# Kernel optimization log

Measured on AMD Instinct MI355X. Metric: run time of the kernel, lower is better.

The kernel has to match this reference:

```python
import jax, jax.numpy as jnp
import numpy as np

HEADS = 20  # SDXL-style: hidden_size 1280 / head_dim 64
IP_SCALE = 1.0


def setup_inputs() -> dict:
    key = jax.random.key(0)
    ks = jax.random.split(key, 12)
    B, Sq, T, C, D, NIP = 4, 4096, 77, 1280, 2048, 16
    s = lambda fan: 1.0 / np.sqrt(fan)
    # post-softmax multiplicative mask: col 0 (sot token) forced to 1, rest a binary spatial mask
    spat = (jax.random.uniform(ks[0], (1, Sq, 1)) < 0.5).astype(jnp.float32)
    attention_mask = jnp.concatenate([jnp.ones((1, Sq, 1)), jnp.tile(spat, (1, 1, T - 1))], axis=-1)
    return {
        "hidden_states": jax.random.normal(ks[1], (B, Sq, C), jnp.float32),
        "encoder_hidden_states": jax.random.normal(ks[2], (B, T, D), jnp.float32),
        "ip_hidden_states": jax.random.normal(ks[3], (B, NIP, D), jnp.float32),
        "attention_mask": attention_mask,
        "Wq": jax.random.normal(ks[4], (C, C), jnp.float32) * s(C),
        "Wk": jax.random.normal(ks[5], (D, C), jnp.float32) * s(D),
        "Wv": jax.random.normal(ks[6], (D, C), jnp.float32) * s(D),
        "Wo": jax.random.normal(ks[7], (C, C), jnp.float32) * s(C),
        "bo": jnp.zeros((C,), jnp.float32),
        "Wk_ip": jax.random.normal(ks[8], (D, C), jnp.float32) * s(D),
        "Wv_ip": jax.random.normal(ks[9], (D, C), jnp.float32) * s(D),
    }


def reference(hidden_states, encoder_hidden_states, ip_hidden_states, attention_mask,
              Wq, Wk, Wv, Wo, bo, Wk_ip, Wv_ip):
    B, Sq, C = hidden_states.shape
    H = HEADS
    d = C // H
    scale = d ** -0.5
    # projections (torch Linear with weights stored [in, out])
    q = (hidden_states @ Wq).reshape(B, Sq, H, d)
    k = (encoder_hidden_states @ Wk).reshape(B, -1, H, d)
    v = (encoder_hidden_states @ Wv).reshape(B, -1, H, d)
    # explicit QK^T softmax, then POST-softmax multiplicative mask (as in get_attention_scores + mask multiply)
    scores = jnp.einsum('bqhd,bkhd->bhqk', q, k) * scale
    probs = jax.nn.softmax(scores, axis=-1)
    probs = probs * attention_mask[:, None, :, :]  # [1,1,Sq,T] broadcast over batch*heads
    out = jnp.einsum('bhqk,bkhd->bqhd', probs, v).reshape(B, Sq, C)
    out = out @ Wo + bo  # to_out[0]; to_out[1] is dropout (identity at eval)
    # IP-adapter stream (single stream, no spatial ip mask): standard SDPA against ip tokens
    k_ip = (ip_hidden_states @ Wk_ip).reshape(B, -1, H, d)
    v_ip = (ip_hidden_states @ Wv_ip).reshape(B, -1, H, d)
    s_ip = jnp.einsum('bqhd,bkhd->bhqk', q, k_ip) * scale
    p_ip = jax.nn.softmax(s_ip, axis=-1)
    ip_out = jnp.einsum('bhqk,bkhd->bqhd', p_ip, v_ip).reshape(B, Sq, C)
    return out + IP_SCALE * ip_out
```

## Files before the change

### kernel.cpp

```cpp
#include <hip/hip_runtime.h>

typedef __attribute__((ext_vector_type(4))) float f32x4;
typedef __attribute__((ext_vector_type(8))) short s16x8;
typedef __attribute__((ext_vector_type(8))) __bf16 bf16x8;
typedef unsigned short u16;

__device__ __forceinline__ u16 f2b(float f) {
  union { float f; unsigned u; } x; x.f = f;
  unsigned r = x.u + 0x7fffu + ((x.u >> 16) & 1u);
  return (u16)(r >> 16);
}
__device__ __forceinline__ float b2f(u16 u) {
  union { unsigned u; float f; } x; x.u = ((unsigned)u) << 16;
  return x.f;
}
__device__ __forceinline__ void gld16(const void* g, void* l) {
  __builtin_amdgcn_global_load_lds(
      (const __attribute__((address_space(1))) unsigned int*)g,
      (__attribute__((address_space(3))) unsigned int*)l, 16, 0, 0);
}
__device__ __forceinline__ f32x4 mfma_bf16(s16x8 a, s16x8 b, f32x4 c) {
  return __builtin_amdgcn_mfma_f32_16x16x32_bf16(
      __builtin_bit_cast(bf16x8, a), __builtin_bit_cast(bf16x8, b), c, 0, 0, 0);
}

#define BAR() asm volatile("s_barrier" ::: "memory")

__global__ void k_convert_all(const float* __restrict__ hs, const float* __restrict__ ehs,
                              const float* __restrict__ iph,
                              u16* __restrict__ hsb, u16* __restrict__ ehsb,
                              u16* __restrict__ ipb) {
  const int n1 = 16384 * 1280 / 4, n2 = 308 * 2048 / 4, n3 = 64 * 2048 / 4;
  int i = blockIdx.x * blockDim.x + threadIdx.x;
  const float* src; u16* dst; int j = i;
  if (i < n1) { src = hs; dst = hsb; }
  else if (i < n1 + n2) { src = ehs; dst = ehsb; j = i - n1; }
  else if (i < n1 + n2 + n3) { src = iph; dst = ipb; j = i - n1 - n2; }
  else return;
  float4 v = ((const float4*)src)[j];
  ushort4 o;
  o.x = f2b(v.x); o.y = f2b(v.y); o.z = f2b(v.z); o.w = f2b(v.w);
  ((ushort4*)dst)[j] = o;
}

__device__ __forceinline__ void transpose_tile(const float* __restrict__ W,
                                               u16* __restrict__ WT, int K, int N) {
  __shared__ float tile[32][33];
  int n0 = blockIdx.x * 32, k0 = blockIdx.y * 32;
  int tx = threadIdx.x & 31, ty = threadIdx.x >> 5;
#pragma unroll
  for (int i = 0; i < 32; i += 8)
    tile[ty + i][tx] = W[(size_t)(k0 + ty + i) * N + n0 + tx];
  __syncthreads();
#pragma unroll
  for (int i = 0; i < 32; i += 8)
    WT[(size_t)(n0 + ty + i) * K + k0 + tx] = f2b(tile[tx][ty + i]);
}

__global__ void k_transpose4(const float* W0, const float* W1, const float* W2,
                             const float* W3, u16* T0, u16* T1, u16* T2, u16* T3,
                             int K, int N) {
  int z = blockIdx.z;
  const float* W = (z == 0) ? W0 : (z == 1) ? W1 : (z == 2) ? W2 : W3;
  u16* T = (z == 0) ? T0 : (z == 1) ? T1 : (z == 2) ? T2 : T3;
  transpose_tile(W, T, K, N);
}
__global__ void k_transpose2(const float* W0, const float* W1, u16* T0, u16* T1,
                             int K, int N) {
  int z = blockIdx.z;
  transpose_tile(z ? W1 : W0, z ? T1 : T0, K, N);
}

__device__ __forceinline__ void gemm_core0(
    const u16* __restrict__ A, const u16* __restrict__ BT,
    int M, int N, int K, u16* __restrict__ outb, int m0, int n0) {
  const int tid = threadIdx.x;
  const int l = tid & 63;
  const int w = tid >> 6;
  const int wr = w >> 1, wc = w & 1;
  __shared__ u16 As[128 * 32];
  __shared__ u16 Bs[128 * 32];
  f32x4 acc[4][4] = {};

  const int o0 = tid * 16;
  const int o1 = o0 + 4096;
  const int ra0 = o0 >> 6, ca0 = (o0 & 63) >> 1;
  const int ra1 = o1 >> 6, ca1 = (o1 & 63) >> 1;
  int ga0 = m0 + ra0; if (ga0 >= M) ga0 = M - 1;
  int ga1 = m0 + ra1; if (ga1 >= M) ga1 = M - 1;
  const u16* Ar0 = A + (size_t)ga0 * K + ca0;
  const u16* Ar1 = A + (size_t)ga1 * K + ca1;
  const u16* Br0 = BT + (size_t)(n0 + ra0) * K + ca0;
  const u16* Br1 = BT + (size_t)(n0 + ra1) * K + ca1;

  for (int k0 = 0; k0 < K; k0 += 32) {
    gld16(Ar0 + k0, &As[o0 >> 1]);
    gld16(Ar1 + k0, &As[o1 >> 1]);
    gld16(Br0 + k0, &Bs[o0 >> 1]);
    gld16(Br1 + k0, &Bs[o1 >> 1]);
    __syncthreads();
    s16x8 af[4], bfr[4];
#pragma unroll
    for (int mi = 0; mi < 4; ++mi)
      af[mi] = *(const s16x8*)&As[(wr * 64 + mi * 16 + (l & 15)) * 32 + (l >> 4) * 8];
#pragma unroll
    for (int ni = 0; ni < 4; ++ni)
      bfr[ni] = *(const s16x8*)&Bs[(wc * 64 + ni * 16 + (l & 15)) * 32 + (l >> 4) * 8];
#pragma unroll
    for (int mi = 0; mi < 4; ++mi)
#pragma unroll
      for (int ni = 0; ni < 4; ++ni)
        acc[mi][ni] = mfma_bf16(af[mi], bfr[ni], acc[mi][ni]);
    __syncthreads();
  }

#pragma unroll
  for (int mi = 0; mi < 4; ++mi) {
    const int mbase = m0 + wr * 64 + mi * 16 + (l >> 4) * 4;
#pragma unroll
    for (int ni = 0; ni < 4; ++ni) {
      const int ncol = n0 + wc * 64 + ni * 16 + (l & 15);
#pragma unroll
      for (int r = 0; r < 4; ++r) {
        int m = mbase + r;
        if (m < M) outb[(size_t)m * N + ncol] = f2b(acc[mi][ni][r]);
      }
    }
  }
}

__global__ __launch_bounds__(256) void k_gemm_small4(
    const u16* __restrict__ ehsb, const u16* __restrict__ ipb,
    const u16* __restrict__ WkT, const u16* __restrict__ WvT,
    const u16* __restrict__ WkipT, const u16* __restrict__ WvipT,
    u16* kbuf, u16* vbuf, u16* kipb, u16* vipb) {
  const int z = blockIdx.z;
  const int M = (z < 2) ? 308 : 64;
  const int m0 = blockIdx.y * 128;
  if (m0 >= M) return;
  const u16* A = (z < 2) ? ehsb : ipb;
  const u16* BT = (z == 0) ? WkT : (z == 1) ? WvT : (z == 2) ? WkipT : WvipT;
  u16* out = (z == 0) ? kbuf : (z == 1) ? vbuf : (z == 2) ? kipb : vipb;
  gemm_core0(A, BT, M, 1280, 2048, out, m0, blockIdx.x * 128);
}

template <int EPI>
__global__ __launch_bounds__(512, 1) void k_gemm256(
    const u16* __restrict__ A, const u16* __restrict__ BT,
    int N, int K, float alpha,
    u16* __restrict__ outb, float* __restrict__ outf,
    const float* __restrict__ bias, const u16* __restrict__ ipadd,
    int nbx) {
  __shared__ u16 lds[73728];
  const int tid = threadIdx.x, l = tid & 63, w = tid >> 6;
  const int lr = l & 15, lg = l >> 4;
  const int wr = w >> 2, wc = w & 3;
  const bool wlo = (w < 4);

  const int nwg = gridDim.x;
  const int q = nwg >> 3, r = nwg & 7;
  const int xcd = blockIdx.x & 7, lid = blockIdx.x >> 3;
  const int wg = (xcd < r) ? (xcd * (q + 1) + lid)
                           : (r * (q + 1) + (xcd - r) * q + lid);
  const int bm0 = (wg / nbx) * 256, bn0 = (wg % nbx) * 320;

  const int srow = tid >> 2;
  const int sslot = ((tid & 3) ^ ((srow >> 1) & 3)) * 8;
  const size_t aO0 = (size_t)(bm0 + srow) * K + sslot;
  const size_t aO1 = aO0 + (size_t)128 * K;
  const size_t bO0 = (size_t)(bn0 + srow) * K + sslot;
  const size_t bO1 = bO0 + (size_t)128 * K;
  const size_t bO2 = bO0 + (size_t)256 * K;
  const int d0 = tid * 8, d1 = (tid + 512) * 8, d2 = (tid + 1024) * 8;

  const int KT = K >> 6;
  f32x4 acc[8][5] = {};
  s16x8 bfv[5], afv[4];

  const int xsw = (lg ^ ((lr >> 1) & 3)) * 8;
  const int aRow = (wr * 128 + lr) * 32 + xsw;
  const int bRow = 32768 + (wc * 80 + lr) * 32 + xsw;

#define STAGE_A(buf, kk, kt)                                           \
  {                                                                    \
    const int base_ = (buf) * 16384 + (kk) * 8192;                     \
    const size_t go_ = (size_t)(kt) * 64 + (kk) * 32;                  \
    gld16(A + aO0 + go_, &lds[base_ + d0]);                            \
    gld16(A + aO1 + go_, &lds[base_ + d1]);                            \
  }
#define STAGE_B(buf, kk, kt)                                           \
  {                                                                    \
    const int base_ = 32768 + (buf) * 20480 + (kk) * 10240;            \
    const size_t go_ = (size_t)(kt) * 64 + (kk) * 32;                  \
    gld16(BT + bO0 + go_, &lds[base_ + d0]);                           \
    gld16(BT + bO1 + go_, &lds[base_ + d1]);                           \
    if (wlo) gld16(BT + bO2 + go_, &lds[base_ + d2]);                  \
  }
#define WAITVM()                                                       \
  {                                                                    \
    if (wlo) asm volatile("s_waitcnt vmcnt(5)" ::: "memory");          \
    else     asm volatile("s_waitcnt vmcnt(4)" ::: "memory");          \
  }
#define WAITVM0() asm volatile("s_waitcnt vmcnt(0)" ::: "memory")

  STAGE_A(0, 0, 0);
  STAGE_B(0, 0, 0);
  STAGE_A(0, 1, 0);
  STAGE_B(0, 1, 0);
  WAITVM();
  BAR();

  int cur = 0;
  for (int j = 0; j < KT; ++j) {
    const int nx = cur ^ 1;
    const int ab = cur * 16384;
    const int bb = cur * 20480;
    const bool pf = (j + 1 < KT);
#pragma unroll
    for (int ni = 0; ni < 5; ++ni)
      bfv[ni] = *(const s16x8*)&lds[bb + bRow + ni * 512];
#pragma unroll
    for (int mi = 0; mi < 4; ++mi)
      afv[mi] = *(const s16x8*)&lds[ab + aRow + mi * 512];
    if (pf) STAGE_A(nx, 0, j + 1);
    __builtin_amdgcn_s_setprio(1);
#pragma unroll
    for (int mi = 0; mi < 4; ++mi)
#pragma unroll
      for (int ni = 0; ni < 5; ++ni)
        acc[mi][ni] = mfma_bf16(afv[mi], bfv[ni], acc[mi][ni]);
    __builtin_amdgcn_s_setprio(0);
    BAR();
#pragma unroll
    for (int mi = 0; mi < 4; ++mi)
      afv[mi] = *(const s16x8*)&lds[ab + aRow + (mi + 4) * 512];
    if (pf) STAGE_B(nx, 0, j + 1);
    __builtin_amdgcn_s_setprio(1);
#pragma unroll
    for (int mi = 0; mi < 4; ++mi)
#pragma unroll
      for (int ni = 0; ni < 5; ++ni)
        acc[mi + 4][ni] = mfma_bf16(afv[mi], bfv[ni], acc[mi + 4][ni]);
    __builtin_amdgcn_s_setprio(0);
    if (pf) { WAITVM(); } else { WAITVM0(); }
    BAR();
#pragma unroll
    for (int ni = 0; ni < 5; ++ni)
      bfv[ni] = *(const s16x8*)&lds[bb + 10240 + bRow + ni * 512];
#pragma unroll
    for (int mi = 0; mi < 4; ++mi)
      afv[mi] = *(const s16x8*)&lds[ab + 8192 + aRow + mi * 512];
    if (pf) STAGE_A(nx, 1, j + 1);
    __builtin_amdgcn_s_setprio(1);
#pragma unroll
    for (int mi = 0; mi < 4; ++mi)
#pragma unroll
      for (int ni = 0; ni < 5; ++ni)
        acc[mi][ni] = mfma_bf16(afv[mi], bfv[ni], acc[mi][ni]);
    __builtin_amdgcn_s_setprio(0);
    BAR();
#pragma unroll
    for (int mi = 0; mi < 4; ++mi)
      afv[mi] = *(const s16x8*)&lds[ab + 8192 + aRow + (mi + 4) * 512];
    if (pf) STAGE_B(nx, 1, j + 1);
    __builtin_amdgcn_s_setprio(1);
#pragma unroll
    for (int mi = 0; mi < 4; ++mi)
#pragma unroll
      for (int ni = 0; ni < 5; ++ni)
        acc[mi + 4][ni] = mfma_bf16(afv[mi], bfv[ni], acc[mi + 4][ni]);
    __builtin_amdgcn_s_setprio(0);
    if (pf) { WAITVM(); } else { WAITVM0(); }
    BAR();
    cur = nx;
  }

  WAITVM0();
  __syncthreads();

  if constexpr (EPI == 0) {
#pragma unroll
    for (int half = 0; half < 2; ++half) {
      if (half) __syncthreads();
      if (wr == half) {
#pragma unroll
        for (int mi = 0; mi < 8; ++mi) {
          const int row = mi * 16 + lg * 4;
#pragma unroll
          for (int ni = 0; ni < 5; ++ni) {
            const int col = wc * 80 + ni * 16 + lr;
#pragma unroll
            for (int rr = 0; rr < 4; ++rr)
              lds[(row + rr) * 320 + col] = f2b(acc[mi][ni][rr] * alpha);
          }
        }
      }
      __syncthreads();
      const int rrow = tid >> 2;
#pragma unroll
      for (int jj = 0; jj < 10; ++jj) {
        const int ch = (tid & 3) + jj * 4;
        *(int4*)(outb + (size_t)(bm0 + half * 128 + rrow) * N + bn0 + ch * 8) =
            *(const int4*)&lds[rrow * 320 + ch * 8];
      }
    }
  } else {
#pragma unroll
    for (int mi = 0; mi < 8; ++mi) {
      const int mrow = bm0 + wr * 128 + mi * 16 + lg * 4;
#pragma unroll
      for (int ni = 0; ni < 5; ++ni) {
        const int ncol = bn0 + wc * 80 + ni * 16 + lr;
#pragma unroll
        for (int rr = 0; rr < 4; ++rr) {
          const size_t idx = (size_t)(mrow + rr) * N + ncol;
          outf[idx] = acc[mi][ni][rr] + bias[ncol] + b2f(ipadd[idx]);
        }
      }
    }
  }
#undef STAGE_A
#undef STAGE_B
#undef WAITVM
#undef WAITVM0
}

__global__ __launch_bounds__(512, 4) void k_attn(
    const u16* __restrict__ Q,
    const u16* __restrict__ Kb,
    const u16* __restrict__ Vb,
    const u16* __restrict__ Kip,
    const u16* __restrict__ Vip,
    const float* __restrict__ mask,
    u16* __restrict__ Oattn,
    u16* __restrict__ Oip) {
  const int qt = blockIdx.x, h = blockIdx.y, b = blockIdx.z;
  const int tid = threadIdx.x, l = tid & 63, w = tid >> 6;
  const int lr = l & 15, lg = l >> 4;
  const int r0 = w * 16;
  const int m0 = b * 4096 + qt * 128;

  __shared__ u16 KV[192][72];
  __shared__ u16 Ps[128][104];
  __shared__ u16 P2s[128][40];

  const u16* qrow = Q + (size_t)(m0 + r0 + lr) * 1280 + h * 64;
  s16x8 aq0 = *(const s16x8*)(qrow + lg * 8);
  s16x8 aq1 = *(const s16x8*)(qrow + 32 + lg * 8);

  for (int s = tid; s < 192 * 8; s += 512) {
    const int row = s >> 3, seg = s & 7;
    int4 v = {0, 0, 0, 0};
    const u16* src = nullptr;
    if (row < 77)       src = Kb  + (size_t)(b * 77 + row) * 1280 + h * 64 + seg * 8;
    else if (row < 80)  src = nullptr;
    else if (row < 96)  src = Kip + (size_t)(b * 16 + row - 80) * 1280 + h * 64 + seg * 8;
    else if (row < 173) src = Vb  + (size_t)(b * 77 + row - 96) * 1280 + h * 64 + seg * 8;
    else if (row < 176) src = nullptr;
    else                src = Vip + (size_t)(b * 16 + row - 176) * 1280 + h * 64 + seg * 8;
    if (src) v = *(const int4*)src;
    *(int4*)&KV[row][(seg ^ ((row >> 3) & 3)) * 8] = v;
  }
  __syncthreads();

  f32x4 sc[5];
  f32x4 sip = {};
#pragma unroll
  for (int t5 = 0; t5 < 6; ++t5) {
    const int trow = t5 * 16 + lr;
    const int qz = (trow >> 3) & 3;
    s16x8 b0 = *(const s16x8*)&KV[trow][(lg ^ qz) * 8];
    s16x8 b1 = *(const s16x8*)&KV[trow][((lg + 4) ^ qz) * 8];
    f32x4 c = {};
    c = mfma_bf16(aq0, b0, c);
    c = mfma_bf16(aq1, b1, c);
    if (t5 < 5) sc[t5] = c; else sip = c;
  }

#pragma unroll
  for (int r = 0; r < 4; ++r) {
    float mx = fmaxf(fmaxf(fmaxf(sc[0][r], sc[1][r]), fmaxf(sc[2][r], sc[3][r])), sc[4][r]);
    mx = fmaxf(mx, __shfl_xor(mx, 1));
    mx = fmaxf(mx, __shfl_xor(mx, 2));
    mx = fmaxf(mx, __shfl_xor(mx, 4));
    mx = fmaxf(mx, __shfl_xor(mx, 8));
    float p[5], sm = 0.f;
#pragma unroll
    for (int t5 = 0; t5 < 5; ++t5) {
      bool valid = (t5 < 4) | (lr < 13);
      p[t5] = valid ? __expf(sc[t5][r] - mx) : 0.f;
      sm += p[t5];
    }
    sm += __shfl_xor(sm, 1);
    sm += __shfl_xor(sm, 2);
    sm += __shfl_xor(sm, 4);
    sm += __shfl_xor(sm, 8);
    const float inv = 1.0f / sm;
    const int row = r0 + lg * 4 + r;
    const int qg = qt * 128 + row;
#pragma unroll
    for (int t5 = 0; t5 < 5; ++t5) {
      int t = t5 * 16 + lr;
      float pf = 0.f;
      if (t < 77) pf = p[t5] * inv * mask[qg * 77 + t];
      Ps[row][t] = f2b(pf);
    }
    Ps[row][80 + lr] = 0;

    float m2 = sip[r];
    m2 = fmaxf(m2, __shfl_xor(m2, 1));
    m2 = fmaxf(m2, __shfl_xor(m2, 2));
    m2 = fmaxf(m2, __shfl_xor(m2, 4));
    m2 = fmaxf(m2, __shfl_xor(m2, 8));
    float pi = __expf(sip[r] - m2);
    float s2 = pi;
    s2 += __shfl_xor(s2, 1);
    s2 += __shfl_xor(s2, 2);
    s2 += __shfl_xor(s2, 4);
    s2 += __shfl_xor(s2, 8);
    P2s[row][lr] = 0;
    P2s[row][16 + lr] = f2b(pi / s2);
  }

  s16x8 ap[3];
#pragma unroll
  for (int ks = 0; ks < 3; ++ks)
    ap[ks] = *(const s16x8*)&Ps[r0 + lr][ks * 32 + lg * 8];
  s16x8 aip = *(const s16x8*)&P2s[r0 + lr][lg * 8];

  f32x4 om[4], oi[4];
#pragma unroll
  for (int nt = 0; nt < 4; ++nt) {
    const int dcol = (nt * 16 + lr) ^ (lg << 3);
    f32x4 o = {};
#pragma unroll
    for (int ks = 0; ks < 3; ++ks) {
      s16x8 bv;
#pragma unroll
      for (int j = 0; j < 8; ++j)
        bv[j] = (short)KV[96 + ks * 32 + lg * 8 + j][dcol];
      o = mfma_bf16(ap[ks], bv, o);
    }
    s16x8 bip;
#pragma unroll
    for (int j = 0; j < 8; ++j)
      bip[j] = (short)KV[160 + lg * 8 + j][dcol];
    f32x4 o2 = {};
    o2 = mfma_bf16(aip, bip, o2);
    om[nt] = o;
    oi[nt] = o2;
  }

  __syncthreads();

  u16 (*Om)[72] = (u16(*)[72]) & KV[0][0];
  u16 (*Oi)[72] = (u16(*)[72]) & Ps[0][0];
#pragma unroll
  for (int nt = 0; nt < 4; ++nt)
#pragma unroll
    for (int r = 0; r < 4; ++r) {
      const int row = r0 + lg * 4 + r;
      const int d = nt * 16 + lr;
      Om[row][d] = f2b(om[nt][r]);
      Oi[row][d] = f2b(oi[nt][r]);
    }
  __syncthreads();

  for (int s = tid; s < 128 * 8; s += 512) {
    const int row = s >> 3, seg = s & 7;
    const size_t g = (size_t)(m0 + row) * 1280 + h * 64 + seg * 8;
    *(int4*)(Oattn + g) = *(const int4*)&Om[row][seg * 8];
    *(int4*)(Oip + g) = *(const int4*)&Oi[row][seg * 8];
  }
}

extern "C" void kernel_launch(void* const* d_in, const int* in_sizes, int n_in,
                              void* d_out, int out_size, void* d_ws, size_t ws_size,
                              hipStream_t stream) {
  (void)in_sizes; (void)n_in; (void)out_size; (void)ws_size;
  const float* hs   = (const float*)d_in[0];
  const float* ehs  = (const float*)d_in[1];
  const float* iph  = (const float*)d_in[2];
  const float* mask = (const float*)d_in[3];
  const float* Wq   = (const float*)d_in[4];
  const float* Wk   = (const float*)d_in[5];
  const float* Wv   = (const float*)d_in[6];
  const float* Wo   = (const float*)d_in[7];
  const float* bo   = (const float*)d_in[8];
  const float* Wkip = (const float*)d_in[9];
  const float* Wvip = (const float*)d_in[10];
  float* out = (float*)d_out;

  char* ws = (char*)d_ws;
  size_t off = 0;
  auto alloc = [&](size_t bytes) {
    char* p = ws + off;
    off += (bytes + 255) & ~(size_t)255;
    return p;
  };
  u16* hsb   = (u16*)alloc(16384ull * 1280 * 2);
  u16* qbuf  = (u16*)alloc(16384ull * 1280 * 2);
  u16* ipout = (u16*)alloc(16384ull * 1280 * 2);
  u16* WqT   = (u16*)alloc(1280ull * 1280 * 2);
  u16* WoT   = (u16*)alloc(1280ull * 1280 * 2);
  u16* WkT   = (u16*)alloc(1280ull * 2048 * 2);
  u16* WvT   = (u16*)alloc(1280ull * 2048 * 2);
  u16* WkipT = (u16*)alloc(1280ull * 2048 * 2);
  u16* WvipT = (u16*)alloc(1280ull * 2048 * 2);
  u16* ehsb  = (u16*)alloc(308ull * 2048 * 2);
  u16* ipb   = (u16*)alloc(64ull * 2048 * 2);
  u16* kbuf  = (u16*)alloc(308ull * 1280 * 2);
  u16* vbuf  = (u16*)alloc(308ull * 1280 * 2);
  u16* kipb  = (u16*)alloc(64ull * 1280 * 2);
  u16* vipb  = (u16*)alloc(64ull * 1280 * 2);

  const int ntot4 = (16384 * 1280 + 308 * 2048 + 64 * 2048) / 4;
  k_convert_all<<<(ntot4 + 255) / 256, 256, 0, stream>>>(hs, ehs, iph, hsb, ehsb, ipb);
  k_transpose4<<<dim3(40, 64, 4), 256, 0, stream>>>(Wk, Wv, Wkip, Wvip,
                                                    WkT, WvT, WkipT, WvipT, 2048, 1280);
  k_transpose2<<<dim3(40, 40, 2), 256, 0, stream>>>(Wq, Wo, WqT, WoT, 1280, 1280);

  k_gemm256<0><<<256, 512, 0, stream>>>(hsb, WqT, 1280, 1280, 0.125f,
                                        qbuf, nullptr, nullptr, nullptr, 4);
  k_gemm_small4<<<dim3(10, 3, 4), 256, 0, stream>>>(ehsb, ipb, WkT, WvT, WkipT, WvipT,
                                                    kbuf, vbuf, kipb, vipb);

  k_attn<<<dim3(32, 20, 4), 512, 0, stream>>>(qbuf, kbuf, vbuf, kipb, vipb, mask,
                                              hsb, ipout);

  k_gemm256<1><<<256, 512, 0, stream>>>(hsb, WoT, 1280, 1280, 1.f,
                                        nullptr, out, bo, ipout, 4);
}
```

Baseline: 266.3 us.

## Deepen GEMM pipeline to four-slot ring with three-ahead prefetch, coalesce epilogue stores

Restructures the GEMM main loop from a double-buffered 64-wide K step (two 32-wide halves) into a four-slot ring of 32-wide K tiles, with prefetch three tiles ahead and vmcnt waits adjusted for the deeper pipeline. This keeps more global loads in flight to hide memory latency, at the cost of one barrier per 32-wide K step and more outstanding loads per wave. It also remaps the bf16 epilogue store so each row is written by eight threads over wider contiguous segments, aiming for better write coalescing.

```diff
diff --git a/kernel.cpp b/kernel.cpp
--- a/kernel.cpp
+++ b/kernel.cpp
@@ -173,7 +173,7 @@
   const size_t bO2 = bO0 + (size_t)256 * K;
   const int d0 = tid * 8, d1 = (tid + 512) * 8, d2 = (tid + 1024) * 8;
 
-  const int KT = K >> 6;
+  const int KT = K >> 5;
   f32x4 acc[8][5] = {};
   s16x8 bfv[5], afv[4];
 
@@ -181,48 +181,52 @@
   const int aRow = (wr * 128 + lr) * 32 + xsw;
   const int bRow = 32768 + (wc * 80 + lr) * 32 + xsw;
 
-#define STAGE_A(buf, kk, kt)                                           \
+#define STAGE_A(slot, kt)                                              \
   {                                                                    \
-    const int base_ = (buf) * 16384 + (kk) * 8192;                     \
-    const size_t go_ = (size_t)(kt) * 64 + (kk) * 32;                  \
+    const int base_ = (slot) * 8192;                                   \
+    const size_t go_ = (size_t)(kt) * 32;                              \
     gld16(A + aO0 + go_, &lds[base_ + d0]);                            \
     gld16(A + aO1 + go_, &lds[base_ + d1]);                            \
   }
-#define STAGE_B(buf, kk, kt)                                           \
+#define STAGE_B(slot, kt)                                              \
   {                                                                    \
-    const int base_ = 32768 + (buf) * 20480 + (kk) * 10240;            \
-    const size_t go_ = (size_t)(kt) * 64 + (kk) * 32;                  \
+    const int base_ = 32768 + (slot) * 10240;                          \
+    const size_t go_ = (size_t)(kt) * 32;                              \
     gld16(BT + bO0 + go_, &lds[base_ + d0]);                           \
     gld16(BT + bO1 + go_, &lds[base_ + d1]);                           \
     if (wlo) gld16(BT + bO2 + go_, &lds[base_ + d2]);                  \
   }
-#define WAITVM()                                                       \
+#define WAIT_DEEP()                                                    \
+  {                                                                    \
+    if (wlo) asm volatile("s_waitcnt vmcnt(10)" ::: "memory");         \
+    else     asm volatile("s_waitcnt vmcnt(8)" ::: "memory");          \
+  }
+#define WAIT_MID()                                                     \
   {                                                                    \
     if (wlo) asm volatile("s_waitcnt vmcnt(5)" ::: "memory");          \
     else     asm volatile("s_waitcnt vmcnt(4)" ::: "memory");          \
   }
 #define WAITVM0() asm volatile("s_waitcnt vmcnt(0)" ::: "memory")
 
-  STAGE_A(0, 0, 0);
-  STAGE_B(0, 0, 0);
-  STAGE_A(0, 1, 0);
-  STAGE_B(0, 1, 0);
-  WAITVM();
+  STAGE_A(0, 0); STAGE_B(0, 0);
+  STAGE_A(1, 1); STAGE_B(1, 1);
+  STAGE_A(2, 2); STAGE_B(2, 2);
+  WAIT_DEEP();
   BAR();
 
-  int cur = 0;
   for (int j = 0; j < KT; ++j) {
-    const int nx = cur ^ 1;
-    const int ab = cur * 16384;
-    const int bb = cur * 20480;
-    const bool pf = (j + 1 < KT);
+    const int slot = j & 3;
+    const int ab = slot * 8192;
+    const int bb = slot * 10240;
+    const bool pf = (j + 3 < KT);
+    const int s3 = (j + 3) & 3;
 #pragma unroll
     for (int ni = 0; ni < 5; ++ni)
       bfv[ni] = *(const s16x8*)&lds[bb + bRow + ni * 512];
 #pragma unroll
     for (int mi = 0; mi < 4; ++mi)
       afv[mi] = *(const s16x8*)&lds[ab + aRow + mi * 512];
-    if (pf) STAGE_A(nx, 0, j + 1);
+    if (pf) STAGE_A(s3, j + 3);
     __builtin_amdgcn_s_setprio(1);
 #pragma unroll
     for (int mi = 0; mi < 4; ++mi)
@@ -234,7 +238,7 @@
 #pragma unroll
     for (int mi = 0; mi < 4; ++mi)
       afv[mi] = *(const s16x8*)&lds[ab + aRow + (mi + 4) * 512];
-    if (pf) STAGE_B(nx, 0, j + 1);
+    if (pf) STAGE_B(s3, j + 3);
     __builtin_amdgcn_s_setprio(1);
 #pragma unroll
     for (int mi = 0; mi < 4; ++mi)
@@ -242,37 +246,10 @@
       for (int ni = 0; ni < 5; ++ni)
         acc[mi + 4][ni] = mfma_bf16(afv[mi], bfv[ni], acc[mi + 4][ni]);
     __builtin_amdgcn_s_setprio(0);
-    if (pf) { WAITVM(); } else { WAITVM0(); }
+    if (pf) { WAIT_DEEP(); }
+    else if (j == KT - 3) { WAIT_MID(); }
+    else { WAITVM0(); }
     BAR();
-#pragma unroll
-    for (int ni = 0; ni < 5; ++ni)
-      bfv[ni] = *(const s16x8*)&lds[bb + 10240 + bRow + ni * 512];
-#pragma unroll
-    for (int mi = 0; mi < 4; ++mi)
-      afv[mi] = *(const s16x8*)&lds[ab + 8192 + aRow + mi * 512];
-    if (pf) STAGE_A(nx, 1, j + 1);
-    __builtin_amdgcn_s_setprio(1);
-#pragma unroll
-    for (int mi = 0; mi < 4; ++mi)
-#pragma unroll
-      for (int ni = 0; ni < 5; ++ni)
-        acc[mi][ni] = mfma_bf16(afv[mi], bfv[ni], acc[mi][ni]);
-    __builtin_amdgcn_s_setprio(0);
-    BAR();
-#pragma unroll
-    for (int mi = 0; mi < 4; ++mi)
-      afv[mi] = *(const s16x8*)&lds[ab + 8192 + aRow + (mi + 4) * 512];
-    if (pf) STAGE_B(nx, 1, j + 1);
-    __builtin_amdgcn_s_setprio(1);
-#pragma unroll
-    for (int mi = 0; mi < 4; ++mi)
-#pragma unroll
-      for (int ni = 0; ni < 5; ++ni)
-        acc[mi + 4][ni] = mfma_bf16(afv[mi], bfv[ni], acc[mi + 4][ni]);
-    __builtin_amdgcn_s_setprio(0);
-    if (pf) { WAITVM(); } else { WAITVM0(); }
-    BAR();
-    cur = nx;
   }
 
   WAITVM0();
@@ -296,13 +273,17 @@
         }
       }
       __syncthreads();
-      const int rrow = tid >> 2;
-#pragma unroll
-      for (int jj = 0; jj < 10; ++jj) {
-        const int ch = (tid & 3) + jj * 4;
-        *(int4*)(outb + (size_t)(bm0 + half * 128 + rrow) * N + bn0 + ch * 8) =
-            *(const int4*)&lds[rrow * 320 + ch * 8];
-      }
+      const int rbase = tid >> 3;
+      const int cseg = tid & 7;
+#pragma unroll
+      for (int rr2 = 0; rr2 < 2; ++rr2)
+#pragma unroll
+        for (int jj = 0; jj < 5; ++jj) {
+          const int row = rr2 * 64 + rbase;
+          const int ch = cseg + jj * 8;
+          *(int4*)(outb + (size_t)(bm0 + half * 128 + row) * N + bn0 + ch * 8) =
+              *(const int4*)&lds[row * 320 + ch * 8];
+        }
     }
   } else {
 #pragma unroll
@@ -321,7 +302,8 @@
   }
 #undef STAGE_A
 #undef STAGE_B
-#undef WAITVM
+#undef WAIT_DEEP
+#undef WAIT_MID
 #undef WAITVM0
 }
 
```

Result: no change. 266.4 us (+0.0%).

## Restructure 256x320 GEMM main loop with 64-wide K slabs and register double-buffering

Applied to the files above, without the earlier changes.

Reworks the large GEMM's K loop. Each iteration now stages a full 64-wide K slab (XOR-swizzled 8-chunk rows) into one of two LDS buffers and issues it once. Fragments are register double-buffered with explicit lgkmcnt waits and sched_barriers, so only one block barrier runs per K step instead of four. The epilogue store pattern is also changed to 8 threads per row for wider coalesced writes. The intent is to cut barrier and synchronisation overhead and overlap LDS reads with MFMA. The trade-off is more register pressure, a full vmcnt(0) wait per step, and 32-bit offsets that could overflow for large operands.

```diff
diff --git a/kernel.cpp b/kernel.cpp
--- a/kernel.cpp
+++ b/kernel.cpp
@@ -155,7 +155,6 @@
   const int tid = threadIdx.x, l = tid & 63, w = tid >> 6;
   const int lr = l & 15, lg = l >> 4;
   const int wr = w >> 2, wc = w & 3;
-  const bool wlo = (w < 4);
 
   const int nwg = gridDim.x;
   const int q = nwg >> 3, r = nwg & 7;
@@ -164,118 +163,108 @@
                            : (r * (q + 1) + (xcd - r) * q + lid);
   const int bm0 = (wg / nbx) * 256, bn0 = (wg % nbx) * 320;
 
-  const int srow = tid >> 2;
-  const int sslot = ((tid & 3) ^ ((srow >> 1) & 3)) * 8;
-  const size_t aO0 = (size_t)(bm0 + srow) * K + sslot;
-  const size_t aO1 = aO0 + (size_t)128 * K;
-  const size_t bO0 = (size_t)(bn0 + srow) * K + sslot;
-  const size_t bO1 = bO0 + (size_t)128 * K;
-  const size_t bO2 = bO0 + (size_t)256 * K;
-  const int d0 = tid * 8, d1 = (tid + 512) * 8, d2 = (tid + 1024) * 8;
+  const int srow = tid >> 3;
+  const int scol = ((tid & 7) ^ (srow & 7)) * 8;
+  const int aOff0 = (bm0 + srow) * K + scol;
+  const int bOff0 = (bn0 + srow) * K + scol;
+  const int dD = tid * 8;
 
   const int KT = K >> 6;
   f32x4 acc[8][5] = {};
-  s16x8 bfv[5], afv[4];
-
-  const int xsw = (lg ^ ((lr >> 1) & 3)) * 8;
-  const int aRow = (wr * 128 + lr) * 32 + xsw;
-  const int bRow = 32768 + (wc * 80 + lr) * 32 + xsw;
-
-#define STAGE_A(buf, kk, kt)                                           \
-  {                                                                    \
-    const int base_ = (buf) * 16384 + (kk) * 8192;                     \
-    const size_t go_ = (size_t)(kt) * 64 + (kk) * 32;                  \
-    gld16(A + aO0 + go_, &lds[base_ + d0]);                            \
-    gld16(A + aO1 + go_, &lds[base_ + d1]);                            \
-  }
-#define STAGE_B(buf, kk, kt)                                           \
-  {                                                                    \
-    const int base_ = 32768 + (buf) * 20480 + (kk) * 10240;            \
-    const size_t go_ = (size_t)(kt) * 64 + (kk) * 32;                  \
-    gld16(BT + bO0 + go_, &lds[base_ + d0]);                           \
-    gld16(BT + bO1 + go_, &lds[base_ + d1]);                           \
-    if (wlo) gld16(BT + bO2 + go_, &lds[base_ + d2]);                  \
-  }
-#define WAITVM()                                                       \
-  {                                                                    \
-    if (wlo) asm volatile("s_waitcnt vmcnt(5)" ::: "memory");          \
-    else     asm volatile("s_waitcnt vmcnt(4)" ::: "memory");          \
-  }
-#define WAITVM0() asm volatile("s_waitcnt vmcnt(0)" ::: "memory")
-
-  STAGE_A(0, 0, 0);
-  STAGE_B(0, 0, 0);
-  STAGE_A(0, 1, 0);
-  STAGE_B(0, 1, 0);
-  WAITVM();
+
+  const int xs0 = (lg ^ (lr & 7)) * 8;
+  const int xs1 = ((4 + lg) ^ (lr & 7)) * 8;
+  const int aR = (wr * 128 + lr) * 64;
+  const int bR = 16384 + (wc * 80 + lr) * 64;
+
+#define SB0() __builtin_amdgcn_sched_barrier(0)
+#define LGKM(n) asm volatile("s_waitcnt lgkmcnt(" #n ")" ::: "memory")
+#define VMW0() asm volatile("s_waitcnt vmcnt(0)" ::: "memory")
+#define STAGE(slotu, kt)                                                \
+  {                                                                     \
+    const int sb_ = (slotu);                                            \
+    const int ko_ = (kt) * 64;                                          \
+    _Pragma("unroll")                                                   \
+    for (int i_ = 0; i_ < 4; ++i_)                                      \
+      gld16(A + aOff0 + i_ * 64 * K + ko_, &lds[sb_ + dD + i_ * 4096]); \
+    _Pragma("unroll")                                                   \
+    for (int i_ = 0; i_ < 5; ++i_)                                      \
+      gld16(BT + bOff0 + i_ * 64 * K + ko_,                             \
+            &lds[sb_ + 16384 + dD + i_ * 4096]);                        \
+  }
+
+  STAGE(0, 0);
+  VMW0();
   BAR();
 
-  int cur = 0;
+  s16x8 afvA[4], afvB[4], bfvA[5], bfvB[5];
   for (int j = 0; j < KT; ++j) {
-    const int nx = cur ^ 1;
-    const int ab = cur * 16384;
-    const int bb = cur * 20480;
+    const int sb = (j & 1) * 36864;
+    const int nsb = 36864 - sb;
     const bool pf = (j + 1 < KT);
 #pragma unroll
+    for (int mi = 0; mi < 4; ++mi)
+      afvA[mi] = *(const s16x8*)&lds[sb + aR + mi * 1024 + xs0];
+#pragma unroll
     for (int ni = 0; ni < 5; ++ni)
-      bfv[ni] = *(const s16x8*)&lds[bb + bRow + ni * 512];
-#pragma unroll
-    for (int mi = 0; mi < 4; ++mi)
-      afv[mi] = *(const s16x8*)&lds[ab + aRow + mi * 512];
-    if (pf) STAGE_A(nx, 0, j + 1);
+      bfvA[ni] = *(const s16x8*)&lds[sb + bR + ni * 1024 + xs0];
+    SB0();
+#pragma unroll
+    for (int mi = 0; mi < 4; ++mi)
+      afvB[mi] = *(const s16x8*)&lds[sb + aR + (mi + 4) * 1024 + xs0];
+    SB0();
+    LGKM(4); SB0();
     __builtin_amdgcn_s_setprio(1);
 #pragma unroll
     for (int mi = 0; mi < 4; ++mi)
 #pragma unroll
       for (int ni = 0; ni < 5; ++ni)
-        acc[mi][ni] = mfma_bf16(afv[mi], bfv[ni], acc[mi][ni]);
+        acc[mi][ni] = mfma_bf16(afvA[mi], bfvA[ni], acc[mi][ni]);
     __builtin_amdgcn_s_setprio(0);
+    SB0();
+#pragma unroll
+    for (int mi = 0; mi < 4; ++mi)
+      afvA[mi] = *(const s16x8*)&lds[sb + aR + mi * 1024 + xs1];
+#pragma unroll
+    for (int ni = 0; ni < 5; ++ni)
+      bfvB[ni] = *(const s16x8*)&lds[sb + bR + ni * 1024 + xs1];
+    SB0();
+    LGKM(9); SB0();
+    __builtin_amdgcn_s_setprio(1);
+#pragma unroll
+    for (int mi = 0; mi < 4; ++mi)
+#pragma unroll
+      for (int ni = 0; ni < 5; ++ni)
+        acc[mi + 4][ni] = mfma_bf16(afvB[mi], bfvA[ni], acc[mi + 4][ni]);
+    __builtin_amdgcn_s_setprio(0);
+    SB0();
+#pragma unroll
+    for (int mi = 0; mi < 4; ++mi)
+      afvB[mi] = *(const s16x8*)&lds[sb + aR + (mi + 4) * 1024 + xs1];
+    SB0();
+    if (pf) STAGE(nsb, j + 1);
+    SB0();
+    LGKM(4); SB0();
+    __builtin_amdgcn_s_setprio(1);
+#pragma unroll
+    for (int mi = 0; mi < 4; ++mi)
+#pragma unroll
+      for (int ni = 0; ni < 5; ++ni)
+        acc[mi][ni] = mfma_bf16(afvA[mi], bfvB[ni], acc[mi][ni]);
+    __builtin_amdgcn_s_setprio(0);
+    SB0();
+    LGKM(0); SB0();
+    __builtin_amdgcn_s_setprio(1);
+#pragma unroll
+    for (int mi = 0; mi < 4; ++mi)
+#pragma unroll
+      for (int ni = 0; ni < 5; ++ni)
+        acc[mi + 4][ni] = mfma_bf16(afvB[mi], bfvB[ni], acc[mi + 4][ni]);
+    __builtin_amdgcn_s_setprio(0);
+    if (pf) VMW0();
     BAR();
-#pragma unroll
-    for (int mi = 0; mi < 4; ++mi)
-      afv[mi] = *(const s16x8*)&lds[ab + aRow + (mi + 4) * 512];
-    if (pf) STAGE_B(nx, 0, j + 1);
-    __builtin_amdgcn_s_setprio(1);
-#pragma unroll
-    for (int mi = 0; mi < 4; ++mi)
-#pragma unroll
-      for (int ni = 0; ni < 5; ++ni)
-        acc[mi + 4][ni] = mfma_bf16(afv[mi], bfv[ni], acc[mi + 4][ni]);
-    __builtin_amdgcn_s_setprio(0);
-    if (pf) { WAITVM(); } else { WAITVM0(); }
-    BAR();
-#pragma unroll
-    for (int ni = 0; ni < 5; ++ni)
-      bfv[ni] = *(const s16x8*)&lds[bb + 10240 + bRow + ni * 512];
-#pragma unroll
-    for (int mi = 0; mi < 4; ++mi)
-      afv[mi] = *(const s16x8*)&lds[ab + 8192 + aRow + mi * 512];
-    if (pf) STAGE_A(nx, 1, j + 1);
-    __builtin_amdgcn_s_setprio(1);
-#pragma unroll
-    for (int mi = 0; mi < 4; ++mi)
-#pragma unroll
-      for (int ni = 0; ni < 5; ++ni)
-        acc[mi][ni] = mfma_bf16(afv[mi], bfv[ni], acc[mi][ni]);
-    __builtin_amdgcn_s_setprio(0);
-    BAR();
-#pragma unroll
-    for (int mi = 0; mi < 4; ++mi)
-      afv[mi] = *(const s16x8*)&lds[ab + 8192 + aRow + (mi + 4) * 512];
-    if (pf) STAGE_B(nx, 1, j + 1);
-    __builtin_amdgcn_s_setprio(1);
-#pragma unroll
-    for (int mi = 0; mi < 4; ++mi)
-#pragma unroll
-      for (int ni = 0; ni < 5; ++ni)
-        acc[mi + 4][ni] = mfma_bf16(afv[mi], bfv[ni], acc[mi + 4][ni]);
-    __builtin_amdgcn_s_setprio(0);
-    if (pf) { WAITVM(); } else { WAITVM0(); }
-    BAR();
-    cur = nx;
-  }
-
-  WAITVM0();
+  }
+
   __syncthreads();
 
   if constexpr (EPI == 0) {
@@ -296,13 +285,17 @@
         }
       }
       __syncthreads();
-      const int rrow = tid >> 2;
-#pragma unroll
-      for (int jj = 0; jj < 10; ++jj) {
-        const int ch = (tid & 3) + jj * 4;
-        *(int4*)(outb + (size_t)(bm0 + half * 128 + rrow) * N + bn0 + ch * 8) =
-            *(const int4*)&lds[rrow * 320 + ch * 8];
-      }
+      const int rbase = tid >> 3;
+      const int cseg = tid & 7;
+#pragma unroll
+      for (int rr2 = 0; rr2 < 2; ++rr2)
+#pragma unroll
+        for (int jj = 0; jj < 5; ++jj) {
+          const int row = rr2 * 64 + rbase;
+          const int ch = cseg + jj * 8;
+          *(int4*)(outb + (size_t)(bm0 + half * 128 + row) * N + bn0 + ch * 8) =
+              *(const int4*)&lds[row * 320 + ch * 8];
+        }
     }
   } else {
 #pragma unroll
@@ -319,10 +312,10 @@
       }
     }
   }
-#undef STAGE_A
-#undef STAGE_B
-#undef WAITVM
-#undef WAITVM0
+#undef SB0
+#undef LGKM
+#undef VMW0
+#undef STAGE
 }
 
 __global__ __launch_bounds__(512, 4) void k_attn(
```

Measured after the change: 265.1 us. About the same (-0.5%).
